# Kernel tuning notes

Hardware: AMD Instinct MI355X
Metric: run time of the kernel (lower is better)

Reference implementation:

```python
import jax, jax.numpy as jnp
import numpy as np

VOCAB, H, E, B, S = 50257, 1024, 1024, 64, 2048


def setup_inputs() -> dict:
    key = jax.random.key(0)
    ks = jax.random.split(key, 12)
    s = 0.02
    return {
        "input_seq": jax.random.randint(ks[0], (B,), 0, VOCAB),
        "last_hidden": jax.random.normal(ks[1], (1, B, H), jnp.float32),
        "last_cell": jax.random.normal(ks[2], (1, B, H), jnp.float32),
        "encoder_outputs": jax.random.normal(ks[3], (S, B, H), jnp.float32),
        "emb_W": jax.random.normal(ks[4], (VOCAB, E), jnp.float32) * s,
        "W_ih": jax.random.normal(ks[5], (4 * H, E), jnp.float32) * s,
        "W_hh": jax.random.normal(ks[6], (4 * H, H), jnp.float32) * s,
        "b_ih": jnp.zeros((4 * H,), jnp.float32),
        "b_hh": jnp.zeros((4 * H,), jnp.float32),
        "concat_W": jax.random.normal(ks[7], (H, 2 * H), jnp.float32) * s,
        "concat_b": jnp.zeros((H,), jnp.float32),
        "out_W": jax.random.normal(ks[8], (VOCAB, H), jnp.float32) * s,
        "out_b": jnp.zeros((VOCAB,), jnp.float32),
    }


def reference(input_seq, last_hidden, last_cell, encoder_outputs,
              emb_W, W_ih, W_hh, b_ih, b_hh,
              concat_W, concat_b, out_W, out_b):
    # Embedding lookup (dropout is identity in eval mode)
    x = emb_W[input_seq]                      # [B, E]
    h0 = last_hidden[0]                       # [B, H]
    c0 = last_cell[0]                         # [B, H]
    # Single LSTM step (PyTorch gate order: i, f, g, o)
    gates = x @ W_ih.T + b_ih + h0 @ W_hh.T + b_hh   # [B, 4H]
    i, f, g, o = jnp.split(gates, 4, axis=-1)
    c = jax.nn.sigmoid(f) * c0 + jax.nn.sigmoid(i) * jnp.tanh(g)
    h = jax.nn.sigmoid(o) * jnp.tanh(c)       # [B, H] == rnn_output
    # 'dot' attention: energies[b, s] = h[b] . enc[s, b]  (vectorized)
    energies = jnp.einsum('bh,sbh->bs', h, encoder_outputs)   # [B, S]
    attn = jax.nn.softmax(energies, axis=1)                   # [B, S]
    context = jnp.einsum('bs,sbh->bh', attn, encoder_outputs) # [B, H]
    concat_out = jnp.tanh(jnp.concatenate([h, context], axis=1) @ concat_W.T + concat_b)
    output = concat_out @ out_W.T + out_b                     # [B, VOCAB]
    return output, h[None], c[None], attn[:, None, :]
```

## Files before the change

### kernel.cpp

```cpp
#include <hip/hip_runtime.h>
#include <hip/hip_bf16.h>
#include <math.h>

#define BB 64
#define HH 1024
#define SS 2048
#define VV 50257

typedef float f32x4 __attribute__((ext_vector_type(4)));
typedef short bf16x8 __attribute__((ext_vector_type(8)));

__device__ __forceinline__ float sigf(float x){ return 1.0f/(1.0f+__expf(-x)); }
__device__ __forceinline__ short f2bf(float f){
  __hip_bfloat16 h = __float2bfloat16(f);
  return __builtin_bit_cast(short, h);
}
__device__ __forceinline__ float bf2f(short s){
  __hip_bfloat16 h = __builtin_bit_cast(__hip_bfloat16, s);
  return __bfloat162float(h);
}

__global__ void k_prep(const int* __restrict__ seq, const float* __restrict__ embW,
                       const float* __restrict__ h0,
                       short* __restrict__ Ahi, short* __restrict__ Alo){
  const int b = blockIdx.x;
  const int k = threadIdx.x * 8;
  const float* src = (k < 1024) ? (embW + (size_t)seq[b]*1024 + k)
                                : (h0 + (size_t)b*1024 + (k - 1024));
  float4 v0 = *(const float4*)src;
  float4 v1 = *(const float4*)(src + 4);
  float v[8] = {v0.x,v0.y,v0.z,v0.w,v1.x,v1.y,v1.z,v1.w};
  bf16x8 hi, lo;
  #pragma unroll
  for (int j = 0; j < 8; ++j) {
    short h = f2bf(v[j]);
    hi[j] = h;
    lo[j] = f2bf(v[j] - bf2f(h));
  }
  *(bf16x8*)(Ahi + (size_t)b*2048 + k) = hi;
  *(bf16x8*)(Alo + (size_t)b*2048 + k) = lo;
}

__global__ __launch_bounds__(256, 3)
void k_gates(const short* __restrict__ Ahi, const short* __restrict__ Alo,
             const float* __restrict__ W_ih, const float* __restrict__ W_hh,
             float* __restrict__ dst)
{
  const int tid = threadIdx.x;
  const int wave = tid >> 6, lane = tid & 63;
  const int r = lane & 15, g = lane >> 4;
  const int nb = blockIdx.x, sk = blockIdx.y;
  const int n0 = nb*128 + wave*32;
  const int kbase = sk*128;
  const float* Wm = (kbase < 1024) ? W_ih : W_hh;
  const int kw = (kbase < 1024) ? kbase : (kbase - 1024);

  f32x4 acc[4][2] = {};

  #pragma unroll
  for (int ks = 0; ks < 4; ++ks) {
    const int kk = kbase + ks*32 + g*8;
    const int ko = kw   + ks*32 + g*8;
    bf16x8 ahi[4], alo[4];
    #pragma unroll
    for (int mf = 0; mf < 4; ++mf) {
      ahi[mf] = *(const bf16x8*)(Ahi + (size_t)(mf*16 + r)*2048 + kk);
      alo[mf] = *(const bf16x8*)(Alo + (size_t)(mf*16 + r)*2048 + kk);
    }
    #pragma unroll
    for (int nf = 0; nf < 2; ++nf) {
      const int n = n0 + nf*16 + r;
      const float* wp = Wm + (size_t)n*1024 + ko;
      float4 w0 = *(const float4*)wp;
      float4 w1 = *(const float4*)(wp + 4);
      float wv[8] = {w0.x,w0.y,w0.z,w0.w,w1.x,w1.y,w1.z,w1.w};
      bf16x8 whi, wlo;
      #pragma unroll
      for (int j = 0; j < 8; ++j) {
        short h = f2bf(wv[j]);
        whi[j] = h;
        wlo[j] = f2bf(wv[j] - bf2f(h));
      }
      #pragma unroll
      for (int mf = 0; mf < 4; ++mf) {
        acc[mf][nf] = __builtin_amdgcn_mfma_f32_16x16x32_bf16(ahi[mf], whi, acc[mf][nf], 0,0,0);
        acc[mf][nf] = __builtin_amdgcn_mfma_f32_16x16x32_bf16(alo[mf], whi, acc[mf][nf], 0,0,0);
        acc[mf][nf] = __builtin_amdgcn_mfma_f32_16x16x32_bf16(ahi[mf], wlo, acc[mf][nf], 0,0,0);
      }
    }
  }

  #pragma unroll
  for (int nf = 0; nf < 2; ++nf) {
    const int n = n0 + nf*16 + r;
    #pragma unroll
    for (int mf = 0; mf < 4; ++mf)
      #pragma unroll
      for (int j = 0; j < 4; ++j)
        dst[((size_t)sk*64 + (mf*16 + g*4 + j))*4096 + n] = acc[mf][nf][j];
  }
}

__global__ void k_rlstm(const float* __restrict__ part, const float* __restrict__ b_ih,
                        const float* __restrict__ b_hh, const float* __restrict__ c0,
                        float* __restrict__ h_out, float* __restrict__ c_out,
                        short* __restrict__ concA, int SK){
  int idx = blockIdx.x*256 + threadIdx.x;
  int b = idx >> 10, k = idx & 1023;
  float gi = b_ih[k]      + b_hh[k];
  float gf = b_ih[1024+k] + b_hh[1024+k];
  float gg = b_ih[2048+k] + b_hh[2048+k];
  float go = b_ih[3072+k] + b_hh[3072+k];
  const float* p = part + (size_t)b*4096 + k;
  for (int s = 0; s < SK; ++s) {
    const float* ps = p + (size_t)s*64*4096;
    gi += ps[0]; gf += ps[1024]; gg += ps[2048]; go += ps[3072];
  }
  float c = sigf(gf)*c0[idx] + sigf(gi)*tanhf(gg);
  float h = sigf(go)*tanhf(c);
  c_out[idx] = c;
  h_out[idx] = h;
  concA[(size_t)b*2048 + k] = f2bf(h);
}

__global__ __launch_bounds__(256)
void k_mfma(const short* __restrict__ A, int lda,
            const float* __restrict__ W1, int ldw,
            float* __restrict__ dst, int N, int Ktot)
{
  const int tid  = threadIdx.x;
  const int wave = tid >> 6, lane = tid & 63;
  const int nb = blockIdx.x, sk = blockIdx.y, SK = gridDim.y;
  const int ksteps = Ktot >> 5;
  const int kps = ksteps / SK;
  const int k0 = sk * kps;
  const int n0 = nb*128 + wave*32;
  const int r = lane & 15, g = lane >> 4;

  f32x4 acc[4][2] = {};

  for (int ks = k0; ks < k0 + kps; ++ks) {
    const int kk = (ks << 5) + g*8;
    bf16x8 af[4];
    #pragma unroll
    for (int mf = 0; mf < 4; ++mf)
      af[mf] = *(const bf16x8*)(A + (size_t)(mf*16 + r)*lda + kk);
    #pragma unroll
    for (int nf = 0; nf < 2; ++nf) {
      const int n = n0 + nf*16 + r;
      const float* wp = W1 + (size_t)n*ldw + kk;
      float4 w0 = *(const float4*)wp;
      float4 w1 = *(const float4*)(wp + 4);
      bf16x8 bfr;
      bfr[0]=f2bf(w0.x); bfr[1]=f2bf(w0.y); bfr[2]=f2bf(w0.z); bfr[3]=f2bf(w0.w);
      bfr[4]=f2bf(w1.x); bfr[5]=f2bf(w1.y); bfr[6]=f2bf(w1.z); bfr[7]=f2bf(w1.w);
      #pragma unroll
      for (int mf = 0; mf < 4; ++mf)
        acc[mf][nf] = __builtin_amdgcn_mfma_f32_16x16x32_bf16(af[mf], bfr, acc[mf][nf], 0, 0, 0);
    }
  }

  #pragma unroll
  for (int nf = 0; nf < 2; ++nf) {
    const int n = n0 + nf*16 + r;
    #pragma unroll
    for (int mf = 0; mf < 4; ++mf)
      #pragma unroll
      for (int j = 0; j < 4; ++j)
        dst[((size_t)sk*64 + (mf*16 + g*4 + j))*N + n] = acc[mf][nf][j];
  }
}

__global__ void k_reduce(const float* __restrict__ part, const float* __restrict__ bias,
                         short* __restrict__ dstb, int N, int SK){
  size_t idx = (size_t)blockIdx.x*256 + threadIdx.x;
  if (idx >= (size_t)64*N) return;
  int b = (int)(idx / N), n = (int)(idx % N);
  float v = bias[n];
  for (int s = 0; s < SK; ++s) v += part[((size_t)s*64 + b)*N + n];
  dstb[(size_t)b*N + n] = f2bf(tanhf(v));
}

__global__ __launch_bounds__(256)
void k_logits3(const short* __restrict__ A, const float* __restrict__ W,
               const float* __restrict__ bias, float* __restrict__ out)
{
  __shared__ short Wl[64 * 256];
  const int tid = threadIdx.x;
  const int wave = tid >> 6, lane = tid & 63;
  const int r = lane & 15, g = lane >> 4;
  const int n0 = blockIdx.x * 64;
  const int myrow = wave*16 + r;

  f32x4 acc[4] = {};

  for (int c = 0; c < 4; ++c) {
    #pragma unroll
    for (int rr = 0; rr < 16; ++rr) {
      const int row = wave*16 + rr;
      const int grow = (n0 + row < VV) ? (n0 + row) : (VV - 1);
      const float4 v = *(const float4*)(W + (size_t)grow*1024 + c*256 + lane*4);
      short4 s;
      s.x = f2bf(v.x); s.y = f2bf(v.y); s.z = f2bf(v.z); s.w = f2bf(v.w);
      *(short4*)((char*)Wl + ((row*512 + lane*8) ^ ((row&7)<<4))) = s;
    }
    __syncthreads();
    const int kc = c*256;
    #pragma unroll 4
    for (int ks = 0; ks < 8; ++ks) {
      const bf16x8 bfr = *(const bf16x8*)((char*)Wl +
            ((myrow*512 + ks*64 + g*16) ^ ((myrow&7)<<4)));
      const int kk = kc + ks*32 + g*8;
      #pragma unroll
      for (int mf = 0; mf < 4; ++mf) {
        const bf16x8 af = *(const bf16x8*)(A + (size_t)(mf*16 + r)*1024 + kk);
        acc[mf] = __builtin_amdgcn_mfma_f32_16x16x32_bf16(af, bfr, acc[mf], 0, 0, 0);
      }
    }
    __syncthreads();
  }

  const int n = n0 + wave*16 + r;
  if (n < VV) {
    const float bv = bias[n];
    #pragma unroll
    for (int mf = 0; mf < 4; ++mf)
      #pragma unroll
      for (int j = 0; j < 4; ++j)
        out[(size_t)(mf*16 + g*4 + j)*VV + n] = acc[mf][j] + bv;
  }
}

__global__ __launch_bounds__(256)
void k_attn_part(const float* __restrict__ h, const float* __restrict__ enc,
                 float* __restrict__ energ, float* __restrict__ mpart,
                 float* __restrict__ lpart, float* __restrict__ ctxpart, int C){
  const int b  = blockIdx.x & 63;
  const int ch = blockIdx.x >> 6;
  const int wave = threadIdx.x >> 6;
  const int lane = threadIdx.x & 63;
  const int rows = SS / C;
  const int rpw  = rows >> 2;
  const int sw = ch*rows + wave*rpw;

  float4 hv0, hv1, hv2, hv3;
  {
    const float* hb = h + (size_t)b*HH + lane*16;
    hv0 = *(const float4*)(hb);   hv1 = *(const float4*)(hb+4);
    hv2 = *(const float4*)(hb+8); hv3 = *(const float4*)(hb+12);
  }
  float m = -INFINITY, l = 0.f;
  float cacc[16];
  #pragma unroll
  for (int j = 0; j < 16; ++j) cacc[j] = 0.f;

  for (int i = 0; i < rpw; i += 2) {
    const float* ep = enc + ((size_t)(sw+i)*BB + b)*HH + lane*16;
    const float* fp = ep + (size_t)BB*HH;
    const float4 e0 = *(const float4*)(ep);
    const float4 e1 = *(const float4*)(ep+4);
    const float4 e2 = *(const float4*)(ep+8);
    const float4 e3 = *(const float4*)(ep+12);
    const float4 f0 = *(const float4*)(fp);
    const float4 f1 = *(const float4*)(fp+4);
    const float4 f2 = *(const float4*)(fp+8);
    const float4 f3 = *(const float4*)(fp+12);
    float p = hv0.x*e0.x + hv0.y*e0.y + hv0.z*e0.z + hv0.w*e0.w
            + hv1.x*e1.x + hv1.y*e1.y + hv1.z*e1.z + hv1.w*e1.w
            + hv2.x*e2.x + hv2.y*e2.y + hv2.z*e2.z + hv2.w*e2.w
            + hv3.x*e3.x + hv3.y*e3.y + hv3.z*e3.z + hv3.w*e3.w;
    float q = hv0.x*f0.x + hv0.y*f0.y + hv0.z*f0.z + hv0.w*f0.w
            + hv1.x*f1.x + hv1.y*f1.y + hv1.z*f1.z + hv1.w*f1.w
            + hv2.x*f2.x + hv2.y*f2.y + hv2.z*f2.z + hv2.w*f2.w
            + hv3.x*f3.x + hv3.y*f3.y + hv3.z*f3.z + hv3.w*f3.w;
    p += __shfl_xor(p, 1);  q += __shfl_xor(q, 1);
    p += __shfl_xor(p, 2);  q += __shfl_xor(q, 2);
    p += __shfl_xor(p, 4);  q += __shfl_xor(q, 4);
    p += __shfl_xor(p, 8);  q += __shfl_xor(q, 8);
    p += __shfl_xor(p, 16); q += __shfl_xor(q, 16);
    p += __shfl_xor(p, 32); q += __shfl_xor(q, 32);
    if (lane == 0) {
      float2 pq; pq.x = p; pq.y = q;
      *(float2*)(energ + (size_t)b*SS + sw + i) = pq;
    }
    const float mn = fmaxf(fmaxf(m, p), q);
    const float sc = __expf(m - mn);
    const float pe = __expf(p - mn);
    const float qe = __expf(q - mn);
    l = l*sc + pe + qe;
    cacc[0] = cacc[0]*sc + pe*e0.x + qe*f0.x;
    cacc[1] = cacc[1]*sc + pe*e0.y + qe*f0.y;
    cacc[2] = cacc[2]*sc + pe*e0.z + qe*f0.z;
    cacc[3] = cacc[3]*sc + pe*e0.w + qe*f0.w;
    cacc[4] = cacc[4]*sc + pe*e1.x + qe*f1.x;
    cacc[5] = cacc[5]*sc + pe*e1.y + qe*f1.y;
    cacc[6] = cacc[6]*sc + pe*e1.z + qe*f1.z;
    cacc[7] = cacc[7]*sc + pe*e1.w + qe*f1.w;
    cacc[8] = cacc[8]*sc + pe*e2.x + qe*f2.x;
    cacc[9] = cacc[9]*sc + pe*e2.y + qe*f2.y;
    cacc[10] = cacc[10]*sc + pe*e2.z + qe*f2.z;
    cacc[11] = cacc[11]*sc + pe*e2.w + qe*f2.w;
    cacc[12] = cacc[12]*sc + pe*e3.x + qe*f3.x;
    cacc[13] = cacc[13]*sc + pe*e3.y + qe*f3.y;
    cacc[14] = cacc[14]*sc + pe*e3.z + qe*f3.z;
    cacc[15] = cacc[15]*sc + pe*e3.w + qe*f3.w;
    m = mn;
  }

  __shared__ float sm[4], sl[4];
  __shared__ float sctx[4][1024];
  if (lane == 0) { sm[wave] = m; sl[wave] = l; }
  __syncthreads();
  const float mg = fmaxf(fmaxf(sm[0], sm[1]), fmaxf(sm[2], sm[3]));
  const float lg = sl[0]*__expf(sm[0]-mg) + sl[1]*__expf(sm[1]-mg)
                 + sl[2]*__expf(sm[2]-mg) + sl[3]*__expf(sm[3]-mg);
  const float scw = __expf(m - mg);
  #pragma unroll
  for (int j = 0; j < 16; ++j) sctx[wave][lane*16 + j] = cacc[j]*scw;
  __syncthreads();
  const int d = threadIdx.x * 4;
  const float4 a0 = *(const float4*)&sctx[0][d];
  const float4 a1 = *(const float4*)&sctx[1][d];
  const float4 a2 = *(const float4*)&sctx[2][d];
  const float4 a3 = *(const float4*)&sctx[3][d];
  float4 rr;
  rr.x = a0.x+a1.x+a2.x+a3.x; rr.y = a0.y+a1.y+a2.y+a3.y;
  rr.z = a0.z+a1.z+a2.z+a3.z; rr.w = a0.w+a1.w+a2.w+a3.w;
  *(float4*)(ctxpart + ((size_t)(b*C + ch))*HH + d) = rr;
  if (threadIdx.x == 0) { mpart[b*C+ch] = mg; lpart[b*C+ch] = lg; }
}

__global__ void k_attn_fin(const float* __restrict__ mpart, const float* __restrict__ lpart,
                           const float* __restrict__ ctxpart, const float* __restrict__ energ,
                           float* __restrict__ attn, short* __restrict__ concA, int C){
  const int b = blockIdx.x, tid = threadIdx.x;
  float m = -INFINITY;
  for (int c = 0; c < C; ++c) m = fmaxf(m, mpart[b*C+c]);
  float l = 0.f;
  for (int c = 0; c < C; ++c) l += lpart[b*C+c] * __expf(mpart[b*C+c] - m);
  const float inv = 1.0f / l;
  float ax = 0.f, ay = 0.f, az = 0.f, aw = 0.f;
  for (int c = 0; c < C; ++c) {
    const float w = __expf(mpart[b*C+c] - m);
    const float* cp = ctxpart + ((size_t)(b*C+c))*HH + tid*4;
    ax += w*cp[0]; ay += w*cp[1]; az += w*cp[2]; aw += w*cp[3];
  }
  ax *= inv; ay *= inv; az *= inv; aw *= inv;
  short* ca = concA + (size_t)b*2048 + 1024 + tid*4;
  ca[0] = f2bf(ax); ca[1] = f2bf(ay); ca[2] = f2bf(az); ca[3] = f2bf(aw);
  for (int j = 0; j < 8; ++j) {
    const int s = j*256 + tid;
    attn[(size_t)b*SS + s] = __expf(energ[(size_t)b*SS + s] - m) * inv;
  }
}

extern "C" void kernel_launch(void* const* d_in, const int* in_sizes, int n_in,
                              void* d_out, int out_size, void* d_ws, size_t ws_size,
                              hipStream_t stream){
  const int*   seq  = (const int*)  d_in[0];
  const float* h0   = (const float*)d_in[1];
  const float* c0   = (const float*)d_in[2];
  const float* enc  = (const float*)d_in[3];
  const float* embW = (const float*)d_in[4];
  const float* W_ih = (const float*)d_in[5];
  const float* W_hh = (const float*)d_in[6];
  const float* b_ih = (const float*)d_in[7];
  const float* b_hh = (const float*)d_in[8];
  const float* cW   = (const float*)d_in[9];
  const float* cb   = (const float*)d_in[10];
  const float* oW   = (const float*)d_in[11];
  const float* ob   = (const float*)d_in[12];
  float* out = (float*)d_out;

  float* ws = (float*)d_ws;
  const size_t o_energ = 0;
  const size_t o_concA = 131072;
  const size_t o_concB = 196608;
  const size_t o_Ahi   = 229376;
  const size_t o_Alo   = 294912;
  const size_t o_mp    = 360448;
  const size_t SKPART  = 4194304;
  int C = 32;
  for (;;) {
    size_t need = (o_mp + (size_t)64*C*2 + (size_t)64*C*1024 + SKPART) * sizeof(float);
    if (need <= ws_size || C == 1) break;
    C >>= 1;
  }
  float* energ   = ws + o_energ;
  short* concA   = (short*)(ws + o_concA);
  short* concB   = (short*)(ws + o_concB);
  short* Ahi     = (short*)(ws + o_Ahi);
  short* Alo     = (short*)(ws + o_Alo);
  float* mpart   = ws + o_mp;
  float* lpart   = mpart + (size_t)64*C;
  float* ctxpart = lpart + (size_t)64*C;
  float* skpart  = ctxpart + (size_t)64*C*1024;

  const size_t o_h = 3216448, o_c = 3281984, o_attn = 3347520;

  k_prep<<<64, 256, 0, stream>>>(seq, embW, h0, Ahi, Alo);
  k_gates<<<dim3(32,16), 256, 0, stream>>>(Ahi, Alo, W_ih, W_hh, skpart);
  k_rlstm<<<256, 256, 0, stream>>>(skpart, b_ih, b_hh, c0, out + o_h, out + o_c,
                                   concA, 16);
  k_attn_part<<<64*C, 256, 0, stream>>>(out + o_h, enc, energ, mpart, lpart, ctxpart, C);
  k_attn_fin<<<64, 256, 0, stream>>>(mpart, lpart, ctxpart, energ, out + o_attn, concA, C);
  k_mfma<<<dim3(8,16), 256, 0, stream>>>(concA, 2048, cW, 2048, skpart, 1024, 2048);
  k_reduce<<<256, 256, 0, stream>>>(skpart, cb, concB, 1024, 16);
  k_logits3<<<786, 256, 0, stream>>>(concB, oW, ob, out);
}
```

Before: 280.6 us.

## Prefetch next W chunk in logits GEMM and coalesce attention encoder loads

The logits kernel now loads the next 256-column chunk of out_W into registers while the MFMA loop works on the current chunk in shared memory, then converts and writes it after a barrier. The aim is to hide global-load latency behind compute. This costs 16 extra float4 registers per thread, which may reduce occupancy. Separately, the attention kernel changes each lane's slice of the hidden dimension from 16 contiguous floats to four float4s strided by 256, so every wave-wide load reads one contiguous 1 KB span. The shared-memory context write is remapped to match.

```diff
diff --git a/kernel.cpp b/kernel.cpp
--- a/kernel.cpp
+++ b/kernel.cpp
@@ -192,19 +192,32 @@
   const int n0 = blockIdx.x * 64;
   const int myrow = wave*16 + r;
 
+#define LOADC(CC, ST) { _Pragma("unroll") \
+    for (int rr = 0; rr < 16; ++rr) { \
+      const int row = wave*16 + rr; \
+      const int grow = (n0 + row < VV) ? (n0 + row) : (VV - 1); \
+      ST[rr] = *(const float4*)(W + (size_t)grow*1024 + (CC)*256 + lane*4); \
+    } }
+#define WRITEC(ST) { _Pragma("unroll") \
+    for (int rr = 0; rr < 16; ++rr) { \
+      const int row = wave*16 + rr; \
+      short4 s4; \
+      s4.x = f2bf(ST[rr].x); s4.y = f2bf(ST[rr].y); \
+      s4.z = f2bf(ST[rr].z); s4.w = f2bf(ST[rr].w); \
+      *(short4*)((char*)Wl + ((row*512 + lane*8) ^ ((row&7)<<4))) = s4; \
+    } }
+
   f32x4 acc[4] = {};
+  {
+    float4 st[16];
+    LOADC(0, st);
+    WRITEC(st);
+  }
+  __syncthreads();
 
   for (int c = 0; c < 4; ++c) {
-    #pragma unroll
-    for (int rr = 0; rr < 16; ++rr) {
-      const int row = wave*16 + rr;
-      const int grow = (n0 + row < VV) ? (n0 + row) : (VV - 1);
-      const float4 v = *(const float4*)(W + (size_t)grow*1024 + c*256 + lane*4);
-      short4 s;
-      s.x = f2bf(v.x); s.y = f2bf(v.y); s.z = f2bf(v.z); s.w = f2bf(v.w);
-      *(short4*)((char*)Wl + ((row*512 + lane*8) ^ ((row&7)<<4))) = s;
-    }
-    __syncthreads();
+    float4 st2[16];
+    if (c < 3) LOADC(c+1, st2);
     const int kc = c*256;
     #pragma unroll 4
     for (int ks = 0; ks < 8; ++ks) {
@@ -218,7 +231,13 @@
       }
     }
     __syncthreads();
-  }
+    if (c < 3) {
+      WRITEC(st2);
+      __syncthreads();
+    }
+  }
+#undef LOADC
+#undef WRITEC
 
   const int n = n0 + wave*16 + r;
   if (n < VV) {
@@ -243,11 +262,13 @@
   const int rpw  = rows >> 2;
   const int sw = ch*rows + wave*rpw;
 
-  float4 hv0, hv1, hv2, hv3;
+  float4 hq0, hq1, hq2, hq3;
   {
-    const float* hb = h + (size_t)b*HH + lane*16;
-    hv0 = *(const float4*)(hb);   hv1 = *(const float4*)(hb+4);
-    hv2 = *(const float4*)(hb+8); hv3 = *(const float4*)(hb+12);
+    const float* hb = h + (size_t)b*HH + lane*4;
+    hq0 = *(const float4*)(hb);
+    hq1 = *(const float4*)(hb + 256);
+    hq2 = *(const float4*)(hb + 512);
+    hq3 = *(const float4*)(hb + 768);
   }
   float m = -INFINITY, l = 0.f;
   float cacc[16];
@@ -255,24 +276,24 @@
   for (int j = 0; j < 16; ++j) cacc[j] = 0.f;
 
   for (int i = 0; i < rpw; i += 2) {
-    const float* ep = enc + ((size_t)(sw+i)*BB + b)*HH + lane*16;
+    const float* ep = enc + ((size_t)(sw+i)*BB + b)*HH + lane*4;
     const float* fp = ep + (size_t)BB*HH;
     const float4 e0 = *(const float4*)(ep);
-    const float4 e1 = *(const float4*)(ep+4);
-    const float4 e2 = *(const float4*)(ep+8);
-    const float4 e3 = *(const float4*)(ep+12);
+    const float4 e1 = *(const float4*)(ep + 256);
+    const float4 e2 = *(const float4*)(ep + 512);
+    const float4 e3 = *(const float4*)(ep + 768);
     const float4 f0 = *(const float4*)(fp);
-    const float4 f1 = *(const float4*)(fp+4);
-    const float4 f2 = *(const float4*)(fp+8);
-    const float4 f3 = *(const float4*)(fp+12);
-    float p = hv0.x*e0.x + hv0.y*e0.y + hv0.z*e0.z + hv0.w*e0.w
-            + hv1.x*e1.x + hv1.y*e1.y + hv1.z*e1.z + hv1.w*e1.w
-            + hv2.x*e2.x + hv2.y*e2.y + hv2.z*e2.z + hv2.w*e2.w
-            + hv3.x*e3.x + hv3.y*e3.y + hv3.z*e3.z + hv3.w*e3.w;
-    float q = hv0.x*f0.x + hv0.y*f0.y + hv0.z*f0.z + hv0.w*f0.w
-            + hv1.x*f1.x + hv1.y*f1.y + hv1.z*f1.z + hv1.w*f1.w
-            + hv2.x*f2.x + hv2.y*f2.y + hv2.z*f2.z + hv2.w*f2.w
-            + hv3.x*f3.x + hv3.y*f3.y + hv3.z*f3.z + hv3.w*f3.w;
+    const float4 f1 = *(const float4*)(fp + 256);
+    const float4 f2 = *(const float4*)(fp + 512);
+    const float4 f3 = *(const float4*)(fp + 768);
+    float p = hq0.x*e0.x + hq0.y*e0.y + hq0.z*e0.z + hq0.w*e0.w
+            + hq1.x*e1.x + hq1.y*e1.y + hq1.z*e1.z + hq1.w*e1.w
+            + hq2.x*e2.x + hq2.y*e2.y + hq2.z*e2.z + hq2.w*e2.w
+            + hq3.x*e3.x + hq3.y*e3.y + hq3.z*e3.z + hq3.w*e3.w;
+    float q = hq0.x*f0.x + hq0.y*f0.y + hq0.z*f0.z + hq0.w*f0.w
+            + hq1.x*f1.x + hq1.y*f1.y + hq1.z*f1.z + hq1.w*f1.w
+            + hq2.x*f2.x + hq2.y*f2.y + hq2.z*f2.z + hq2.w*f2.w
+            + hq3.x*f3.x + hq3.y*f3.y + hq3.z*f3.z + hq3.w*f3.w;
     p += __shfl_xor(p, 1);  q += __shfl_xor(q, 1);
     p += __shfl_xor(p, 2);  q += __shfl_xor(q, 2);
     p += __shfl_xor(p, 4);  q += __shfl_xor(q, 4);
@@ -288,16 +309,16 @@
     const float pe = __expf(p - mn);
     const float qe = __expf(q - mn);
     l = l*sc + pe + qe;
-    cacc[0] = cacc[0]*sc + pe*e0.x + qe*f0.x;
-    cacc[1] = cacc[1]*sc + pe*e0.y + qe*f0.y;
-    cacc[2] = cacc[2]*sc + pe*e0.z + qe*f0.z;
-    cacc[3] = cacc[3]*sc + pe*e0.w + qe*f0.w;
-    cacc[4] = cacc[4]*sc + pe*e1.x + qe*f1.x;
-    cacc[5] = cacc[5]*sc + pe*e1.y + qe*f1.y;
-    cacc[6] = cacc[6]*sc + pe*e1.z + qe*f1.z;
-    cacc[7] = cacc[7]*sc + pe*e1.w + qe*f1.w;
-    cacc[8] = cacc[8]*sc + pe*e2.x + qe*f2.x;
-    cacc[9] = cacc[9]*sc + pe*e2.y + qe*f2.y;
+    cacc[0]  = cacc[0]*sc  + pe*e0.x + qe*f0.x;
+    cacc[1]  = cacc[1]*sc  + pe*e0.y + qe*f0.y;
+    cacc[2]  = cacc[2]*sc  + pe*e0.z + qe*f0.z;
+    cacc[3]  = cacc[3]*sc  + pe*e0.w + qe*f0.w;
+    cacc[4]  = cacc[4]*sc  + pe*e1.x + qe*f1.x;
+    cacc[5]  = cacc[5]*sc  + pe*e1.y + qe*f1.y;
+    cacc[6]  = cacc[6]*sc  + pe*e1.z + qe*f1.z;
+    cacc[7]  = cacc[7]*sc  + pe*e1.w + qe*f1.w;
+    cacc[8]  = cacc[8]*sc  + pe*e2.x + qe*f2.x;
+    cacc[9]  = cacc[9]*sc  + pe*e2.y + qe*f2.y;
     cacc[10] = cacc[10]*sc + pe*e2.z + qe*f2.z;
     cacc[11] = cacc[11]*sc + pe*e2.w + qe*f2.w;
     cacc[12] = cacc[12]*sc + pe*e3.x + qe*f3.x;
@@ -316,7 +337,12 @@
                  + sl[2]*__expf(sm[2]-mg) + sl[3]*__expf(sm[3]-mg);
   const float scw = __expf(m - mg);
   #pragma unroll
-  for (int j = 0; j < 16; ++j) sctx[wave][lane*16 + j] = cacc[j]*scw;
+  for (int j = 0; j < 4; ++j) {
+    float4 v;
+    v.x = cacc[j*4+0]*scw; v.y = cacc[j*4+1]*scw;
+    v.z = cacc[j*4+2]*scw; v.w = cacc[j*4+3]*scw;
+    *(float4*)&sctx[wave][j*256 + lane*4] = v;
+  }
   __syncthreads();
   const int d = threadIdx.x * 4;
   const float4 a0 = *(const float4*)&sctx[0][d];
```

After: 294.8 us. +5.1%, slower.
